# Kernel tuning notes

Hardware: AMD Instinct MI355X
Metric: run time of the kernel (lower is better)

## Reference

```python
import jax, jax.numpy as jnp
import numpy as np

B, N, D = 4, 2048, 1024
H = 16
DH = D // H


def setup_inputs() -> dict:
    key = jax.random.key(0)
    ks = jax.random.split(key, 9)
    s_in = 1.0 / np.sqrt(D)
    x = jax.random.normal(ks[0], (B, N, D), dtype=jnp.float32)
    Wq = jax.random.uniform(ks[1], (D, D), jnp.float32, -s_in, s_in)
    bq = jax.random.uniform(ks[2], (D,), jnp.float32, -s_in, s_in)
    Wk = jax.random.uniform(ks[3], (D, D), jnp.float32, -s_in, s_in)
    bk = jax.random.uniform(ks[4], (D,), jnp.float32, -s_in, s_in)
    Wv = jax.random.uniform(ks[5], (D, D), jnp.float32, -s_in, s_in)
    bv = jax.random.uniform(ks[6], (D,), jnp.float32, -s_in, s_in)
    Wo = jax.random.uniform(ks[7], (D, D), jnp.float32, -s_in, s_in)
    bo = jax.random.uniform(ks[8], (D,), jnp.float32, -s_in, s_in)
    return {"x": x, "Wq": Wq, "bq": bq, "Wk": Wk, "bk": bk,
            "Wv": Wv, "bv": bv, "Wo": Wo, "bo": bo}


def reference(x, Wq, bq, Wk, bk, Wv, bv, Wo, bo):
    b, n, d = x.shape
    q = (x @ Wq + bq).reshape(b, n, H, DH)  # (b, n, h, dh)
    k = (x @ Wk + bk).reshape(b, n, H, DH)
    v = (x @ Wv + bv).reshape(b, n, H, DH)
    scale = 1.0 / jnp.sqrt(jnp.asarray(DH, x.dtype))
    scores = jnp.einsum("bqhd,bkhd->bhqk", q, k) * scale  # (b, h, n, n)
    # valid = arange(1..n) per query => causal mask: key index < valid[q] = q+1
    causal = jnp.arange(n)[None, :] <= jnp.arange(n)[:, None]  # (n_q, n_k)
    scores = jnp.where(causal[None, None, :, :], scores, -jnp.inf)
    weights = jax.nn.softmax(scores, axis=-1)
    out = jnp.einsum("bhqk,bkhd->bqhd", weights, v).reshape(b, n, d)
    return out @ Wo + bo
```

## Files before the change

kernel.cpp:

```cpp
#include <hip/hip_runtime.h>
#include <hip/hip_bf16.h>
#include <math.h>

namespace {
constexpr int B_ = 4, N_ = 2048, D_ = 1024, H_ = 16, DH_ = 64;
constexpr int M_ = B_ * N_;
}

typedef __bf16 bf16x8 __attribute__((ext_vector_type(8)));
typedef __bf16 bf16x4 __attribute__((ext_vector_type(4)));
typedef float  f32x4  __attribute__((ext_vector_type(4)));

__device__ inline void async_copy16(const void* g, void* l) {
    __builtin_amdgcn_global_load_lds(
        (const __attribute__((address_space(1))) unsigned int*)g,
        (__attribute__((address_space(3))) unsigned int*)l, 16, 0, 0);
}

__device__ inline float fast_exp2(float x) {
#if __has_builtin(__builtin_amdgcn_exp2f)
    return __builtin_amdgcn_exp2f(x);
#else
    return exp2f(x);
#endif
}

__device__ inline int swz(int row, int c) {
    return c ^ (row & 3) ^ ((row >> 2) & 3);
}

__global__ __launch_bounds__(256) void cast_x(
        const float* __restrict__ x, __bf16* __restrict__ xb)
{
    const size_t i = ((size_t)blockIdx.x * 256 + threadIdx.x) * 8;
    const float4 a = *reinterpret_cast<const float4*>(x + i);
    const float4 b = *reinterpret_cast<const float4*>(x + i + 4);
    bf16x8 o;
    o[0] = (__bf16)a.x; o[1] = (__bf16)a.y; o[2] = (__bf16)a.z; o[3] = (__bf16)a.w;
    o[4] = (__bf16)b.x; o[5] = (__bf16)b.y; o[6] = (__bf16)b.z; o[7] = (__bf16)b.w;
    *reinterpret_cast<bf16x8*>(xb + i) = o;
}

__global__ __launch_bounds__(256) void cast_w(
        const float* __restrict__ Wq, const float* __restrict__ Wk,
        const float* __restrict__ Wv, const float* __restrict__ Wo,
        __bf16* __restrict__ wqkvt, __bf16* __restrict__ wot)
{
    __shared__ float t[64][65];
    const int z = blockIdx.z;
    const float* W = (z == 0) ? Wq : (z == 1) ? Wk : (z == 2) ? Wv : Wo;
    __bf16* dst = (z < 3) ? (wqkvt + (size_t)z * D_ * D_) : wot;
    const int k0 = blockIdx.x * 64, n0 = blockIdx.y * 64;
    const int tid = threadIdx.x;
    #pragma unroll
    for (int p = 0; p < 16; ++p) {
        const int idx = p * 256 + tid;
        const int r = idx >> 6, c = idx & 63;
        t[r][c] = W[(size_t)(k0 + r) * D_ + n0 + c];
    }
    __syncthreads();
    #pragma unroll
    for (int p = 0; p < 16; ++p) {
        const int idx = p * 256 + tid;
        const int r = idx >> 6, c = idx & 63;
        dst[(size_t)(n0 + r) * D_ + k0 + c] = (__bf16)t[c][r];
    }
}

__global__ __launch_bounds__(512, 2) void qkv_mfma(
        const __bf16* __restrict__ A, const __bf16* __restrict__ Bt,
        const float* __restrict__ bq, const float* __restrict__ bk,
        const float* __restrict__ bv,
        __bf16* __restrict__ qo, __bf16* __restrict__ ko, __bf16* __restrict__ vo)
{
    __shared__ __align__(16) __bf16 As[2][256 * 64];
    __shared__ __align__(16) __bf16 Bs[2][256 * 64];
    const int tid = threadIdx.x;
    const int w = tid >> 6, lane = tid & 63;
    const int l15 = lane & 15, quad = lane >> 4;
    const int wr = w >> 2, wc = w & 3;
    const int tm = blockIdx.x * 256;
    const int bn = blockIdx.y * 256;

    const __bf16* Ag = A + (size_t)tm * D_;
    const __bf16* Bg = Bt + (size_t)bn * D_;

    f32x4 acc[8][4] = {};

    auto stageAh = [&](int t, int half) {
        const int slot = t & 1;
        const int k0 = t * 64;
        #pragma unroll
        for (int s = 0; s < 2; ++s) {
            const int li = s * 512 + tid;
            const int rl = li >> 3, cs = li & 7;
            const int r = half * 64 + rl + (rl & 64);
            const int csrc = cs ^ (r & 7);
            async_copy16(Ag + (size_t)r * D_ + k0 + csrc * 8,
                         &As[slot][(r * 8 + cs) * 8]);
        }
    };
    auto stageBh = [&](int t, int par) {
        const int slot = t & 1;
        const int k0 = t * 64;
        #pragma unroll
        for (int s = 0; s < 2; ++s) {
            const int li = s * 512 + tid;
            const int cl = li >> 3, cs = li & 7;
            const int col = (cl & 31) + ((cl >> 5) << 6) + par * 32;
            const int csrc = cs ^ (col & 7);
            async_copy16(Bg + (size_t)col * D_ + k0 + csrc * 8,
                         &Bs[slot][(col * 8 + cs) * 8]);
        }
    };

#define QKV_PHASE(Ab, Bb, qq, STAGE_STMT, WAIT_STMT)                          \
    {                                                                         \
        const int ar0 = wr * 128 + ((qq) >> 1) * 64;                          \
        const int bc0 = wc * 64 + ((qq) & 1) * 32;                            \
        bf16x8 af[4][2], bfv[2][2];                                           \
        _Pragma("unroll")                                                     \
        for (int fr = 0; fr < 4; ++fr) {                                      \
            const int row = ar0 + fr * 16 + l15;                              \
            _Pragma("unroll")                                                 \
            for (int ks = 0; ks < 2; ++ks)                                    \
                af[fr][ks] = *reinterpret_cast<const bf16x8*>(                \
                    (Ab) + row * 64 + (((ks * 4 + quad) ^ (row & 7)) * 8));   \
        }                                                                     \
        _Pragma("unroll")                                                     \
        for (int nc = 0; nc < 2; ++nc) {                                      \
            const int col = bc0 + nc * 16 + l15;                              \
            _Pragma("unroll")                                                 \
            for (int ks = 0; ks < 2; ++ks)                                    \
                bfv[nc][ks] = *reinterpret_cast<const bf16x8*>(               \
                    (Bb) + col * 64 + (((ks * 4 + quad) ^ (col & 7)) * 8));   \
        }                                                                     \
        STAGE_STMT;                                                           \
        WAIT_STMT;                                                            \
        asm volatile("s_barrier" ::: "memory");                               \
        __builtin_amdgcn_s_setprio(1);                                        \
        _Pragma("unroll")                                                     \
        for (int fr = 0; fr < 4; ++fr)                                        \
            _Pragma("unroll")                                                 \
            for (int nc = 0; nc < 2; ++nc) {                                  \
                f32x4 c = acc[((qq) >> 1) * 4 + fr][((qq) & 1) * 2 + nc];     \
                c = __builtin_amdgcn_mfma_f32_16x16x32_bf16(af[fr][0], bfv[nc][0], c, 0, 0, 0); \
                c = __builtin_amdgcn_mfma_f32_16x16x32_bf16(af[fr][1], bfv[nc][1], c, 0, 0, 0); \
                acc[((qq) >> 1) * 4 + fr][((qq) & 1) * 2 + nc] = c;           \
            }                                                                 \
        __builtin_amdgcn_s_setprio(0);                                        \
        asm volatile("s_barrier" ::: "memory");                               \
    }

    stageAh(0, 0); stageAh(0, 1); stageBh(0, 0); stageBh(0, 1);
    stageAh(1, 0); stageBh(1, 0);
    asm volatile("s_waitcnt vmcnt(4)" ::: "memory");
    asm volatile("s_barrier" ::: "memory");

    for (int i = 0; i < 8; ++i) {
        const int T1 = 2 * i + 1;
        const bool more = (i < 7);
        const __bf16* A0 = As[0]; const __bf16* B0 = Bs[0];
        const __bf16* A1 = As[1]; const __bf16* B1 = Bs[1];

        QKV_PHASE(A0, B0, 0, stageAh(T1, 1), ((void)0));
        QKV_PHASE(A0, B0, 1, stageBh(T1, 1), ((void)0));
        QKV_PHASE(A0, B0, 2, if (more) stageAh(T1 + 1, 0), ((void)0));
        QKV_PHASE(A0, B0, 3, if (more) stageBh(T1 + 1, 0),
                  if (more) { asm volatile("s_waitcnt vmcnt(4)" ::: "memory"); }
                  else      { asm volatile("s_waitcnt vmcnt(0)" ::: "memory"); });
        QKV_PHASE(A1, B1, 0, if (more) stageAh(T1 + 1, 1), ((void)0));
        QKV_PHASE(A1, B1, 1, if (more) stageBh(T1 + 1, 1), ((void)0));
        QKV_PHASE(A1, B1, 2, if (more) stageAh(T1 + 2, 0), ((void)0));
        QKV_PHASE(A1, B1, 3, if (more) stageBh(T1 + 2, 0),
                  if (more) { asm volatile("s_waitcnt vmcnt(4)" ::: "memory"); });
    }
#undef QKV_PHASE

    const int z = blockIdx.y >> 2;
    const float* bias = (z == 0) ? bq : (z == 1) ? bk : bv;
    const int ysec = blockIdx.y & 3;
    const int h = ysec * 4 + wc;
    float bcol[4];
    #pragma unroll
    for (int nc = 0; nc < 4; ++nc) bcol[nc] = bias[h * 64 + nc * 16 + l15];
    const int gr0 = tm + wr * 128;

    if (z < 2) {
        __bf16* dst = (z == 0) ? qo : ko;
        const float sc = (z == 0) ? 0.125f * 1.44269504f : 1.0f;
        #pragma unroll
        for (int mr = 0; mr < 8; ++mr)
            #pragma unroll
            for (int i = 0; i < 4; ++i) {
                const int gr = gr0 + mr * 16 + quad * 4 + i;
                const int b = gr >> 11, tok = gr & (N_ - 1);
                __bf16* row = dst + ((size_t)(b * H_ + h) * N_ + tok) * DH_;
                #pragma unroll
                for (int nc = 0; nc < 4; ++nc)
                    row[nc * 16 + l15] = (__bf16)((acc[mr][nc][i] + bcol[nc]) * sc);
            }
    } else {
        #pragma unroll
        for (int mr = 0; mr < 8; ++mr) {
            const int gr = gr0 + mr * 16 + quad * 4;
            const int b = gr >> 11, tok = gr & (N_ - 1);
            #pragma unroll
            for (int nc = 0; nc < 4; ++nc) {
                const int dh = nc * 16 + l15;
                bf16x4 pv;
                #pragma unroll
                for (int i = 0; i < 4; ++i)
                    pv[i] = (__bf16)(acc[mr][nc][i] + bcol[nc]);
                *reinterpret_cast<bf16x4*>(
                    vo + ((size_t)(b * H_ + h) * DH_ + dh) * N_ + tok) = pv;
            }
        }
    }
}

__global__ __launch_bounds__(256) void out_mfma(
        const __bf16* __restrict__ A, const __bf16* __restrict__ Bt,
        const float* __restrict__ bias, float* __restrict__ out)
{
    __shared__ __align__(16) __bf16 As[128 * 32];
    __shared__ __align__(16) __bf16 Bs[128 * 32];
    const int tid = threadIdx.x;
    const int w = tid >> 6, lane = tid & 63;
    const int l15 = lane & 15, quad = lane >> 4;
    const int tm = blockIdx.x * 128;
    const int tn = blockIdx.y * 128;

    f32x4 acc[4][4] = {};

    for (int k0 = 0; k0 < D_; k0 += 32) {
        __syncthreads();
        #pragma unroll
        for (int it = 0; it < 2; ++it) {
            const int c = it * 256 + tid;
            const int r = c >> 2, pc = c & 3;
            const int lc = swz(r, pc);
            async_copy16(A + (size_t)(tm + r) * D_ + k0 + lc * 8, As + c * 8);
            async_copy16(Bt + (size_t)(tn + r) * D_ + k0 + lc * 8, Bs + c * 8);
        }
        __syncthreads();

        bf16x8 af[4], bfr[4];
        #pragma unroll
        for (int t = 0; t < 4; ++t) {
            const int row = (w >> 1) * 64 + t * 16 + l15;
            af[t] = *reinterpret_cast<const bf16x8*>(
                As + (row * 4 + swz(row, quad)) * 8);
            const int col = (w & 1) * 64 + t * 16 + l15;
            bfr[t] = *reinterpret_cast<const bf16x8*>(
                Bs + (col * 4 + swz(col, quad)) * 8);
        }
        #pragma unroll
        for (int mt = 0; mt < 4; ++mt)
            #pragma unroll
            for (int nt = 0; nt < 4; ++nt)
                acc[mt][nt] = __builtin_amdgcn_mfma_f32_16x16x32_bf16(
                    af[mt], bfr[nt], acc[mt][nt], 0, 0, 0);
    }

    const int col0 = tn + (w & 1) * 64;
    float bcol[4];
    #pragma unroll
    for (int nt = 0; nt < 4; ++nt) bcol[nt] = bias[col0 + nt * 16 + l15];
    const int gr0 = tm + (w >> 1) * 64;
    #pragma unroll
    for (int mt = 0; mt < 4; ++mt)
        #pragma unroll
        for (int i = 0; i < 4; ++i) {
            const int gr = gr0 + mt * 16 + quad * 4 + i;
            float* row = out + (size_t)gr * D_;
            #pragma unroll
            for (int nt = 0; nt < 4; ++nt)
                row[col0 + nt * 16 + l15] = acc[mt][nt][i] + bcol[nt];
        }
}

__global__ __launch_bounds__(256, 4) void attn(
        const __bf16* __restrict__ Q, const __bf16* __restrict__ K,
        const __bf16* __restrict__ Vt, __bf16* __restrict__ ctx)
{
    const int blk = blockIdx.x;
    const int bh = blk & 63;
    const int qb = ((blk >> 6) + bh) & 15;
    const int tid = threadIdx.x;
    const int w = tid >> 6, lane = tid & 63;
    const int l15 = lane & 15, quad = lane >> 4;
    const int qt0 = qb * 128;

    __shared__ __align__(16) __bf16 Ks[64 * 64];
    __shared__ __align__(16) __bf16 Vs[64 * 64];
    __shared__ __align__(16) __bf16 Ps[4][2][16 * 72];

    bf16x8 bqf[2][2];
    #pragma unroll
    for (int qc = 0; qc < 2; ++qc) {
        const size_t base = ((size_t)bh * N_ + qt0 + w * 32 + qc * 16 + l15) * DH_;
        bqf[qc][0] = *reinterpret_cast<const bf16x8*>(Q + base + quad * 8);
        bqf[qc][1] = *reinterpret_cast<const bf16x8*>(Q + base + 32 + quad * 8);
    }

    f32x4 acc[2][4] = {};
    float l_lane[2] = {0.f, 0.f};

    const __bf16* Kg = K + (size_t)bh * N_ * DH_;
    const __bf16* Vg = Vt + (size_t)bh * DH_ * N_;
    const int nkb = 2 * qb + 2;
    const int sr = lane >> 3;
    const int sc = lane & 7;

    for (int kb = 0; kb < nkb; ++kb) {
        __syncthreads();
        #pragma unroll
        for (int j = 0; j < 2; ++j) {
            const int r = j * 32 + w * 8 + sr;
            const int cl = sc ^ (r & 7);
            async_copy16(Kg + (size_t)(kb * 64 + r) * DH_ + cl * 8,
                         &Ks[(j * 256 + tid) * 8]);
            async_copy16(Vg + (size_t)r * N_ + kb * 64 + cl * 8,
                         &Vs[(j * 256 + tid) * 8]);
        }
        __syncthreads();

        f32x4 st[2][4];
        __builtin_amdgcn_s_setprio(1);
        #pragma unroll
        for (int ct = 0; ct < 4; ++ct) {
            const int row = ct * 16 + l15;
            const bf16x8 ka0 = *reinterpret_cast<const bf16x8*>(
                &Ks[(row * 8 + (quad ^ (row & 7))) * 8]);
            const bf16x8 ka1 = *reinterpret_cast<const bf16x8*>(
                &Ks[(row * 8 + ((quad + 4) ^ (row & 7))) * 8]);
            #pragma unroll
            for (int qc = 0; qc < 2; ++qc) {
                f32x4 t = {};
                t = __builtin_amdgcn_mfma_f32_16x16x32_bf16(ka0, bqf[qc][0], t, 0, 0, 0);
                t = __builtin_amdgcn_mfma_f32_16x16x32_bf16(ka1, bqf[qc][1], t, 0, 0, 0);
                st[qc][ct] = t;
            }
        }
        __builtin_amdgcn_s_setprio(0);
        if (kb >= 2 * qb) {
            #pragma unroll
            for (int qc = 0; qc < 2; ++qc) {
                const int q_glob = qt0 + w * 32 + qc * 16 + l15;
                #pragma unroll
                for (int ct = 0; ct < 4; ++ct)
                    #pragma unroll
                    for (int i = 0; i < 4; ++i) {
                        const int k_glob = kb * 64 + ct * 16 + quad * 4 + i;
                        if (k_glob > q_glob) st[qc][ct][i] = -INFINITY;
                    }
            }
        }

        #pragma unroll
        for (int qc = 0; qc < 2; ++qc) {
            float rs = 0.f;
            #pragma unroll
            for (int ct = 0; ct < 4; ++ct) {
                bf16x4 pk;
                #pragma unroll
                for (int i = 0; i < 4; ++i) {
                    const float p = fast_exp2(st[qc][ct][i]);
                    rs += p;
                    pk[i] = (__bf16)p;
                }
                *reinterpret_cast<bf16x4*>(
                    &Ps[w][qc][l15 * 72 + ct * 16 + quad * 4]) = pk;
            }
            l_lane[qc] += rs;
        }

        bf16x8 pa0[2], pa1[2];
        #pragma unroll
        for (int qc = 0; qc < 2; ++qc) {
            pa0[qc] = *reinterpret_cast<const bf16x8*>(
                &Ps[w][qc][l15 * 72 + quad * 8]);
            pa1[qc] = *reinterpret_cast<const bf16x8*>(
                &Ps[w][qc][l15 * 72 + 32 + quad * 8]);
        }
        __builtin_amdgcn_s_setprio(1);
        #pragma unroll
        for (int ct = 0; ct < 4; ++ct) {
            const int row = ct * 16 + l15;
            const bf16x8 vb0 = *reinterpret_cast<const bf16x8*>(
                &Vs[(row * 8 + (quad ^ (row & 7))) * 8]);
            const bf16x8 vb1 = *reinterpret_cast<const bf16x8*>(
                &Vs[(row * 8 + ((quad + 4) ^ (row & 7))) * 8]);
            #pragma unroll
            for (int qc = 0; qc < 2; ++qc) {
                f32x4 t = acc[qc][ct];
                t = __builtin_amdgcn_mfma_f32_16x16x32_bf16(pa0[qc], vb0, t, 0, 0, 0);
                t = __builtin_amdgcn_mfma_f32_16x16x32_bf16(pa1[qc], vb1, t, 0, 0, 0);
                acc[qc][ct] = t;
            }
        }
        __builtin_amdgcn_s_setprio(0);
    }

    const int b = bh >> 4, h = bh & 15;
    #pragma unroll
    for (int qc = 0; qc < 2; ++qc) {
        float r = l_lane[qc];
        r += __shfl_xor(r, 16);
        r += __shfl_xor(r, 32);
        const float linv = 1.0f / r;
        float lT[4];
        #pragma unroll
        for (int i = 0; i < 4; ++i) lT[i] = __shfl(linv, quad * 4 + i);
        #pragma unroll
        for (int i = 0; i < 4; ++i) {
            const int row = qt0 + w * 32 + qc * 16 + quad * 4 + i;
            __bf16* dst = ctx + ((size_t)b * N_ + row) * D_ + h * DH_;
            #pragma unroll
            for (int ct = 0; ct < 4; ++ct)
                dst[ct * 16 + l15] = (__bf16)(acc[qc][ct][i] * lT[i]);
        }
    }
}

extern "C" void kernel_launch(void* const* d_in, const int* in_sizes, int n_in,
                              void* d_out, int out_size, void* d_ws, size_t ws_size,
                              hipStream_t stream) {
    const float* x  = (const float*)d_in[0];
    const float* Wq = (const float*)d_in[1];
    const float* bq = (const float*)d_in[2];
    const float* Wk = (const float*)d_in[3];
    const float* bk = (const float*)d_in[4];
    const float* Wv = (const float*)d_in[5];
    const float* bv = (const float*)d_in[6];
    const float* Wo = (const float*)d_in[7];
    const float* bo = (const float*)d_in[8];
    float* out = (float*)d_out;

    __bf16* xb    = (__bf16*)d_ws;
    __bf16* wqkvt = xb + (size_t)M_ * D_;
    __bf16* wot   = wqkvt + (size_t)3 * D_ * D_;
    __bf16* q     = wot + (size_t)D_ * D_;
    __bf16* k     = q + (size_t)M_ * D_;
    __bf16* vt    = k + (size_t)M_ * D_;
    __bf16* ctx   = vt + (size_t)M_ * D_;

    cast_x<<<dim3(M_ * D_ / (256 * 8)), 256, 0, stream>>>(x, xb);
    cast_w<<<dim3(16, 16, 4), 256, 0, stream>>>(Wq, Wk, Wv, Wo, wqkvt, wot);
    qkv_mfma<<<dim3(M_ / 256, 3 * D_ / 256), 512, 0, stream>>>(
        xb, wqkvt, bq, bk, bv, q, k, vt);
    attn<<<dim3(1024), 256, 0, stream>>>(q, k, vt, ctx);
    out_mfma<<<dim3(M_ / 128, D_ / 128), 256, 0, stream>>>(ctx, wot, bo, out);
}
```

Baseline: 264.3 us.

## Split QKV GEMM phases along K and reuse B fragments across row halves

Each phase of the QKV projection GEMM main loop now handles one 32-wide K slice for a full 64-column strip. B fragments are loaded once and reused across both 64-row halves, rather than each phase loading two K slices for a 32-column quadrant. This cuts LDS reads of B and reorders the asynchronous global-to-LDS staging so the pipeline keeps fewer loads in flight (vmcnt 2 instead of 4). A sched_barrier is added after the prologue. The risk is a shorter prefetch distance, which could expose memory latency.

```diff
diff --git a/kernel.cpp b/kernel.cpp
--- a/kernel.cpp
+++ b/kernel.cpp
@@ -114,26 +114,23 @@
         }
     };
 
-#define QKV_PHASE(Ab, Bb, qq, STAGE_STMT, WAIT_STMT)                          \
+#define QKV_PHASE(Ab, Bb, KS, HALF, READB, STAGE_STMT, WAIT_STMT)             \
     {                                                                         \
-        const int ar0 = wr * 128 + ((qq) >> 1) * 64;                          \
-        const int bc0 = wc * 64 + ((qq) & 1) * 32;                            \
-        bf16x8 af[4][2], bfv[2][2];                                           \
+        const int ar0 = wr * 128 + (HALF) * 64;                               \
+        bf16x8 af[4];                                                         \
         _Pragma("unroll")                                                     \
         for (int fr = 0; fr < 4; ++fr) {                                      \
             const int row = ar0 + fr * 16 + l15;                              \
+            af[fr] = *reinterpret_cast<const bf16x8*>(                        \
+                (Ab) + row * 64 + ((((KS) * 4 + quad) ^ (row & 7)) * 8));     \
+        }                                                                     \
+        if (READB) {                                                          \
             _Pragma("unroll")                                                 \
-            for (int ks = 0; ks < 2; ++ks)                                    \
-                af[fr][ks] = *reinterpret_cast<const bf16x8*>(                \
-                    (Ab) + row * 64 + (((ks * 4 + quad) ^ (row & 7)) * 8));   \
-        }                                                                     \
-        _Pragma("unroll")                                                     \
-        for (int nc = 0; nc < 2; ++nc) {                                      \
-            const int col = bc0 + nc * 16 + l15;                              \
-            _Pragma("unroll")                                                 \
-            for (int ks = 0; ks < 2; ++ks)                                    \
-                bfv[nc][ks] = *reinterpret_cast<const bf16x8*>(               \
-                    (Bb) + col * 64 + (((ks * 4 + quad) ^ (col & 7)) * 8));   \
+            for (int nc = 0; nc < 4; ++nc) {                                  \
+                const int col = wc * 64 + nc * 16 + l15;                      \
+                bfv[nc] = *reinterpret_cast<const bf16x8*>(                   \
+                    (Bb) + col * 64 + ((((KS) * 4 + quad) ^ (col & 7)) * 8)); \
+            }                                                                 \
         }                                                                     \
         STAGE_STMT;                                                           \
         WAIT_STMT;                                                            \
@@ -142,38 +139,36 @@
         _Pragma("unroll")                                                     \
         for (int fr = 0; fr < 4; ++fr)                                        \
             _Pragma("unroll")                                                 \
-            for (int nc = 0; nc < 2; ++nc) {                                  \
-                f32x4 c = acc[((qq) >> 1) * 4 + fr][((qq) & 1) * 2 + nc];     \
-                c = __builtin_amdgcn_mfma_f32_16x16x32_bf16(af[fr][0], bfv[nc][0], c, 0, 0, 0); \
-                c = __builtin_amdgcn_mfma_f32_16x16x32_bf16(af[fr][1], bfv[nc][1], c, 0, 0, 0); \
-                acc[((qq) >> 1) * 4 + fr][((qq) & 1) * 2 + nc] = c;           \
-            }                                                                 \
+            for (int nc = 0; nc < 4; ++nc)                                    \
+                acc[(HALF) * 4 + fr][nc] =                                    \
+                    __builtin_amdgcn_mfma_f32_16x16x32_bf16(                  \
+                        af[fr], bfv[nc], acc[(HALF) * 4 + fr][nc], 0, 0, 0);  \
         __builtin_amdgcn_s_setprio(0);                                        \
         asm volatile("s_barrier" ::: "memory");                               \
     }
 
     stageAh(0, 0); stageAh(0, 1); stageBh(0, 0); stageBh(0, 1);
-    stageAh(1, 0); stageBh(1, 0);
-    asm volatile("s_waitcnt vmcnt(4)" ::: "memory");
+    stageAh(1, 0);
+    asm volatile("s_waitcnt vmcnt(2)" ::: "memory");
     asm volatile("s_barrier" ::: "memory");
+    __builtin_amdgcn_sched_barrier(0);
 
     for (int i = 0; i < 8; ++i) {
-        const int T1 = 2 * i + 1;
         const bool more = (i < 7);
         const __bf16* A0 = As[0]; const __bf16* B0 = Bs[0];
         const __bf16* A1 = As[1]; const __bf16* B1 = Bs[1];
-
-        QKV_PHASE(A0, B0, 0, stageAh(T1, 1), ((void)0));
-        QKV_PHASE(A0, B0, 1, stageBh(T1, 1), ((void)0));
-        QKV_PHASE(A0, B0, 2, if (more) stageAh(T1 + 1, 0), ((void)0));
-        QKV_PHASE(A0, B0, 3, if (more) stageBh(T1 + 1, 0),
-                  if (more) { asm volatile("s_waitcnt vmcnt(4)" ::: "memory"); }
+        bf16x8 bfv[4];
+        QKV_PHASE(A0, B0, 0, 0, true,  stageAh(2 * i + 1, 1), ((void)0));
+        QKV_PHASE(A0, B0, 0, 1, false, stageBh(2 * i + 1, 0), ((void)0));
+        QKV_PHASE(A0, B0, 1, 0, true,  stageBh(2 * i + 1, 1), ((void)0));
+        QKV_PHASE(A0, B0, 1, 1, false, if (more) stageAh(2 * i + 2, 0),
+                  if (more) { asm volatile("s_waitcnt vmcnt(2)" ::: "memory"); }
                   else      { asm volatile("s_waitcnt vmcnt(0)" ::: "memory"); });
-        QKV_PHASE(A1, B1, 0, if (more) stageAh(T1 + 1, 1), ((void)0));
-        QKV_PHASE(A1, B1, 1, if (more) stageBh(T1 + 1, 1), ((void)0));
-        QKV_PHASE(A1, B1, 2, if (more) stageAh(T1 + 2, 0), ((void)0));
-        QKV_PHASE(A1, B1, 3, if (more) stageBh(T1 + 2, 0),
-                  if (more) { asm volatile("s_waitcnt vmcnt(4)" ::: "memory"); });
+        QKV_PHASE(A1, B1, 0, 0, true,  if (more) stageBh(2 * i + 2, 0), ((void)0));
+        QKV_PHASE(A1, B1, 0, 1, false, if (more) stageBh(2 * i + 2, 1), ((void)0));
+        QKV_PHASE(A1, B1, 1, 0, true,  if (more) stageAh(2 * i + 2, 1), ((void)0));
+        QKV_PHASE(A1, B1, 1, 1, false, if (more) stageAh(2 * i + 3, 0),
+                  if (more) { asm volatile("s_waitcnt vmcnt(2)" ::: "memory"); });
     }
 #undef QKV_PHASE
 
```

New measurement: 256.9 us. 1.03x faster.
